# Optimization experiments

Hardware: AMD Instinct MI355X
Metric: run time of the kernel (lower is better)

Reference implementation:

```python
import jax, jax.numpy as jnp
import numpy as np

ZETA = 1.1
GAMMA = -0.1

B, F, D = 1024, 32, 128


def setup_inputs() -> dict:
    key = jax.random.key(0)
    k1, k2 = jax.random.split(key)
    feature = jax.random.normal(k1, (B, F, D), dtype=jnp.float32)
    # nn.Parameter init: normal(mean=0, std=0.001)
    matrix = jax.random.normal(k2, (F, F, D, D), dtype=jnp.float32) * 0.001
    return {"feature": feature, "matrix": matrix}


def reference(feature, matrix):
    # feature: [B, F, D]; matrix (logAlpha of hard-concrete gate): [F, F, D, D]
    nF = matrix.shape[0]
    # strict upper-triangular pair mask over (i, j)
    mask = jnp.triu(jnp.ones((nF, nF), dtype=feature.dtype), k=1)
    # deterministic (eval-mode) hard-concrete gate: stretch + clamp
    s = jax.nn.sigmoid(matrix)
    z = jnp.clip(s * (ZETA - GAMMA) + GAMMA, 0.0, 1.0)
    l0_out = mask[:, :, None, None] * z  # [F, F, D, D]
    # out[b,i,j] = f_i^T Z_ij f_j  == sum_{d,e} f[b,i,d] * Z[i,j,d,e] * f[b,j,e]
    # (faithful to: (f[:, :, None, :, None] @ f[:, None, :, None, :]) * Z, summed over (d, e))
    out = jnp.einsum('bid,ijde,bje->bij', feature, l0_out, feature)
    return out
```

## Files before the change

kernel.cpp:

```cpp
#include <hip/hip_runtime.h>

#define B_SZ 1024
#define F_SZ 32
#define D_SZ 128
#define FD   (F_SZ * D_SZ)
#define NPAIR 496

typedef __bf16 bf16x8 __attribute__((ext_vector_type(8)));
typedef __bf16 bf16x4 __attribute__((ext_vector_type(4)));
typedef float floatx4 __attribute__((ext_vector_type(4)));
typedef unsigned short u16x8 __attribute__((ext_vector_type(8)));

__device__ __forceinline__ unsigned short f2bf(float f) {
  unsigned u = __float_as_uint(f);
  u += 0x7fffu + ((u >> 16) & 1u);
  return (unsigned short)(u >> 16);
}

__device__ __forceinline__ float bf2f(unsigned short h) {
  return __uint_as_float(((unsigned)h) << 16);
}

__device__ __forceinline__ void gload_lds16(const void* g, void* l) {
  __builtin_amdgcn_global_load_lds(
      (const __attribute__((address_space(1))) unsigned int*)g,
      (__attribute__((address_space(3))) unsigned int*)l,
      16, 0, 0);
}

__global__ __launch_bounds__(256)
void prep_kernel(const float* __restrict__ feat, const float* __restrict__ mat,
                 unsigned short* __restrict__ featHi, unsigned short* __restrict__ featLo,
                 unsigned short* __restrict__ ZT, float* __restrict__ out) {
  const int bid = blockIdx.x, t = threadIdx.x;
  __shared__ unsigned short tr[128 * 72];

  if (bid < 2 * NPAIR) {
    const int pid = bid >> 1, h = bid & 1, d0 = h * 64;
    int p = pid, i = 0;
    while (p >= F_SZ - 1 - i) { p -= F_SZ - 1 - i; ++i; }
    const int j = i + 1 + p;
    const float* zp = mat + (((size_t)i * F_SZ + j) * (size_t)(D_SZ * D_SZ));
    #pragma unroll
    for (int it = 0; it < 8; ++it) {
      int idx4 = it * 256 + t;
      int dl = idx4 >> 5, e4 = (idx4 & 31) * 4;
      const float4 v = *(const float4*)(zp + (size_t)(d0 + dl) * D_SZ + e4);
      float zs[4] = {v.x, v.y, v.z, v.w};
      #pragma unroll
      for (int c = 0; c < 4; ++c) {
        float s = 1.0f / (1.0f + __expf(-zs[c]));
        float z = fminf(1.0f, fmaxf(0.0f, fmaf(s, 1.2f, -0.1f)));
        tr[(e4 + c) * 72 + dl] = f2bf(z);
      }
    }
    __syncthreads();
    #pragma unroll
    for (int it = 0; it < 4; ++it) {
      int G = it * 256 + t;
      int e = G >> 3, gl = G & 7;
      int gs = gl ^ (e & 7);
      u16x8 v = *(const u16x8*)&tr[e * 72 + gs * 8];
      *(u16x8*)&ZT[(size_t)pid * (D_SZ * D_SZ) + e * 128 + d0 + gl * 8] = v;
    }
  } else if (bid < 2 * NPAIR + 1024) {
    int idx = (bid - 2 * NPAIR) * 256 + t;
    const float4* f4 = (const float4*)feat + (size_t)idx * 4;
    #pragma unroll
    for (int q = 0; q < 2; ++q) {
      float4 a = f4[q * 2], b = f4[q * 2 + 1];
      float vs[8] = {a.x, a.y, a.z, a.w, b.x, b.y, b.z, b.w};
      u16x8 hi, lo;
      #pragma unroll
      for (int c = 0; c < 8; ++c) {
        unsigned short hh = f2bf(vs[c]);
        hi[c] = hh;
        lo[c] = f2bf(vs[c] - bf2f(hh));
      }
      *(u16x8*)&featHi[(size_t)idx * 16 + q * 8] = hi;
      *(u16x8*)&featLo[(size_t)idx * 16 + q * 8] = lo;
    }
  } else {
    int idx = (bid - (2 * NPAIR + 1024)) * 256 + t;
    float4* o4 = (float4*)out + (size_t)idx * 4;
    float4 z = {0.f, 0.f, 0.f, 0.f};
    o4[0] = z; o4[1] = z; o4[2] = z; o4[3] = z;
  }
}

__global__ __launch_bounds__(256, 3)
void interaction_pair_kernel(const unsigned short* __restrict__ featHi,
                             const unsigned short* __restrict__ featLo,
                             const unsigned short* __restrict__ ZT,
                             float* __restrict__ out) {
  __shared__ unsigned short sZ[128 * 128];
  __shared__ unsigned short sW[4 * 2048];

  const int t    = threadIdx.x;
  const int w    = t >> 6;
  const int lane = t & 63;
  const int l15  = lane & 15;
  const int quad = lane >> 4;
  const int swz  = (l15 & 7) << 4;

  const int pid   = blockIdx.x >> 3;
  const int split = blockIdx.x & 7;
  int p = pid, i = 0;
  while (p >= F_SZ - 1 - i) { p -= F_SZ - 1 - i; ++i; }
  const int j = i + 1 + p;

  {
    const char* src = (const char*)(ZT + (size_t)pid * (D_SZ * D_SZ));
    #pragma unroll
    for (int it = 0; it < 8; ++it) {
      int off = it * 4096 + w * 1024;
      gload_lds16(src + off + lane * 16, (char*)sZ + off);
    }
  }
  __syncthreads();

  const int rbase = split * 128 + w * 32;

  floatx4 acc[8][2];
  #pragma unroll
  for (int m = 0; m < 8; ++m) {
    acc[m][0] = (floatx4){0.f, 0.f, 0.f, 0.f};
    acc[m][1] = (floatx4){0.f, 0.f, 0.f, 0.f};
  }

  #pragma unroll
  for (int k0 = 0; k0 < 4; ++k0) {
    const int dq = k0 * 32 + quad * 8;
    bf16x8 b0f = *(const bf16x8*)&featHi[(size_t)(rbase +      l15) * FD + i * D_SZ + dq];
    bf16x8 b1f = *(const bf16x8*)&featHi[(size_t)(rbase + 16 + l15) * FD + i * D_SZ + dq];
    #pragma unroll
    for (int m = 0; m < 8; ++m) {
      const int e = m * 16 + l15;
      bf16x8 za = *(const bf16x8*)((const char*)sZ + e * 256 + ((2 * dq) ^ swz));
      acc[m][0] = __builtin_amdgcn_mfma_f32_16x16x32_bf16(za, b0f, acc[m][0], 0, 0, 0);
      acc[m][1] = __builtin_amdgcn_mfma_f32_16x16x32_bf16(za, b1f, acc[m][1], 0, 0, 0);
    }
  }

  char* wb = (char*)(sW + w * 2048);
  #pragma unroll
  for (int n = 0; n < 2; ++n) {
    #pragma unroll
    for (int m = 0; m < 8; ++m) {
      floatx4 c = acc[m][n];
      bf16x4 v = {(__bf16)c[0], (__bf16)c[1], (__bf16)c[2], (__bf16)c[3]};
      const int e0 = m * 16 + quad * 4;
      *(bf16x4*)(wb + l15 * 256 + ((2 * e0) ^ swz)) = v;
    }
    const int row = rbase + n * 16 + l15;
    const unsigned short* fj_h = featHi + (size_t)row * FD + j * D_SZ;
    const unsigned short* fj_l = featLo + (size_t)row * FD + j * D_SZ;
    floatx4 g = (floatx4){0.f, 0.f, 0.f, 0.f};
    #pragma unroll
    for (int k0 = 0; k0 < 4; ++k0) {
      bf16x8 wf = *(const bf16x8*)(wb + l15 * 256 + ((k0 * 64 + quad * 16) ^ swz));
      bf16x8 ah = *(const bf16x8*)(fj_h + k0 * 32 + quad * 8);
      bf16x8 al = *(const bf16x8*)(fj_l + k0 * 32 + quad * 8);
      g = __builtin_amdgcn_mfma_f32_16x16x32_bf16(ah, wf, g, 0, 0, 0);
      g = __builtin_amdgcn_mfma_f32_16x16x32_bf16(al, wf, g, 0, 0, 0);
    }
    if ((l15 >> 2) == quad) {
      const int r = l15 & 3;
      float val = g[r];
      out[(size_t)row * (F_SZ * F_SZ) + (size_t)i * F_SZ + j] = val;
    }
  }
}

extern "C" void kernel_launch(void* const* d_in, const int* in_sizes, int n_in,
                              void* d_out, int out_size, void* d_ws, size_t ws_size,
                              hipStream_t stream) {
  const float* feat = (const float*)d_in[0];
  const float* mat  = (const float*)d_in[1];
  float* out = (float*)d_out;

  unsigned short* featHi = (unsigned short*)d_ws;
  unsigned short* featLo = featHi + (size_t)B_SZ * F_SZ * D_SZ;
  unsigned short* ZT     = featLo + (size_t)B_SZ * F_SZ * D_SZ;

  const int prep_grid = 2 * NPAIR + 1024 + 256;
  prep_kernel<<<dim3(prep_grid), dim3(256), 0, stream>>>(feat, mat, featHi, featLo, ZT, out);
  interaction_pair_kernel<<<dim3(NPAIR * 8), dim3(256), 0, stream>>>(featHi, featLo, ZT, out);
}
```

Before: 158.1 us.

## Keep Z tile in registers across batch passes and finish dot product in fp32

Each block now covers 512 batch rows in four passes instead of 128, and the whole 128x128 bf16 Z tile is loaded once from LDS into registers and reused across passes. The second stage no longer rounds the intermediate to bf16, writes it to LDS and runs split hi/lo MFMAs. Instead it dots the fp32 MFMA accumulators with the fp32 feature_j directly, then reduces across lanes with shuffles. This drops the featLo workspace and the intermediate LDS buffer, at the cost of far more VGPRs (occupancy bound lowered to 2) and fewer blocks (992).

```diff
diff --git a/kernel.cpp b/kernel.cpp
--- a/kernel.cpp
+++ b/kernel.cpp
@@ -3,11 +3,10 @@
 #define B_SZ 1024
 #define F_SZ 32
 #define D_SZ 128
-#define FD   (F_SZ * D_SZ)
+#define FD   4096
 #define NPAIR 496
 
 typedef __bf16 bf16x8 __attribute__((ext_vector_type(8)));
-typedef __bf16 bf16x4 __attribute__((ext_vector_type(4)));
 typedef float floatx4 __attribute__((ext_vector_type(4)));
 typedef unsigned short u16x8 __attribute__((ext_vector_type(8)));
 
@@ -17,8 +16,8 @@
   return (unsigned short)(u >> 16);
 }
 
-__device__ __forceinline__ float bf2f(unsigned short h) {
-  return __uint_as_float(((unsigned)h) << 16);
+__device__ __forceinline__ bf16x8 as_bf16x8(floatx4 v) {
+  union { floatx4 f; bf16x8 b; } u; u.f = v; return u.b;
 }
 
 __device__ __forceinline__ void gload_lds16(const void* g, void* l) {
@@ -30,7 +29,7 @@
 
 __global__ __launch_bounds__(256)
 void prep_kernel(const float* __restrict__ feat, const float* __restrict__ mat,
-                 unsigned short* __restrict__ featHi, unsigned short* __restrict__ featLo,
+                 unsigned short* __restrict__ featB,
                  unsigned short* __restrict__ ZT, float* __restrict__ out) {
   const int bid = blockIdx.x, t = threadIdx.x;
   __shared__ unsigned short tr[128 * 72];
@@ -70,15 +69,10 @@
     for (int q = 0; q < 2; ++q) {
       float4 a = f4[q * 2], b = f4[q * 2 + 1];
       float vs[8] = {a.x, a.y, a.z, a.w, b.x, b.y, b.z, b.w};
-      u16x8 hi, lo;
+      u16x8 hi;
       #pragma unroll
-      for (int c = 0; c < 8; ++c) {
-        unsigned short hh = f2bf(vs[c]);
-        hi[c] = hh;
-        lo[c] = f2bf(vs[c] - bf2f(hh));
-      }
-      *(u16x8*)&featHi[(size_t)idx * 16 + q * 8] = hi;
-      *(u16x8*)&featLo[(size_t)idx * 16 + q * 8] = lo;
+      for (int c = 0; c < 8; ++c) hi[c] = f2bf(vs[c]);
+      *(u16x8*)&featB[(size_t)idx * 16 + q * 8] = hi;
     }
   } else {
     int idx = (bid - (2 * NPAIR + 1024)) * 256 + t;
@@ -88,13 +82,12 @@
   }
 }
 
-__global__ __launch_bounds__(256, 3)
-void interaction_pair_kernel(const unsigned short* __restrict__ featHi,
-                             const unsigned short* __restrict__ featLo,
+__global__ __launch_bounds__(256, 2)
+void interaction_pair_kernel(const float* __restrict__ feat,
+                             const unsigned short* __restrict__ featB,
                              const unsigned short* __restrict__ ZT,
                              float* __restrict__ out) {
   __shared__ unsigned short sZ[128 * 128];
-  __shared__ unsigned short sW[4 * 2048];
 
   const int t    = threadIdx.x;
   const int w    = t >> 6;
@@ -103,8 +96,8 @@
   const int quad = lane >> 4;
   const int swz  = (l15 & 7) << 4;
 
-  const int pid   = blockIdx.x >> 3;
-  const int split = blockIdx.x & 7;
+  const int pid   = blockIdx.x >> 1;
+  const int split = blockIdx.x & 1;
   int p = pid, i = 0;
   while (p >= F_SZ - 1 - i) { p -= F_SZ - 1 - i; ++i; }
   const int j = i + 1 + p;
@@ -119,55 +112,52 @@
   }
   __syncthreads();
 
-  const int rbase = split * 128 + w * 32;
+  floatx4 zr[4][8];
+  #pragma unroll
+  for (int k0 = 0; k0 < 4; ++k0)
+    #pragma unroll
+    for (int m = 0; m < 8; ++m)
+      zr[k0][m] = *(const floatx4*)((const char*)sZ + (m * 16 + l15) * 256 +
+                                    ((k0 * 64 + quad * 16) ^ swz));
+  #pragma unroll
+  for (int k0 = 0; k0 < 4; ++k0)
+    #pragma unroll
+    for (int m = 0; m < 8; ++m)
+      asm volatile("" : "+v"(zr[k0][m]));
 
-  floatx4 acc[8][2];
-  #pragma unroll
-  for (int m = 0; m < 8; ++m) {
-    acc[m][0] = (floatx4){0.f, 0.f, 0.f, 0.f};
-    acc[m][1] = (floatx4){0.f, 0.f, 0.f, 0.f};
-  }
+  #pragma unroll 1
+  for (int pass = 0; pass < 4; ++pass) {
+    const int rbase = split * 512 + pass * 128 + w * 32;
 
-  #pragma unroll
-  for (int k0 = 0; k0 < 4; ++k0) {
-    const int dq = k0 * 32 + quad * 8;
-    bf16x8 b0f = *(const bf16x8*)&featHi[(size_t)(rbase +      l15) * FD + i * D_SZ + dq];
-    bf16x8 b1f = *(const bf16x8*)&featHi[(size_t)(rbase + 16 + l15) * FD + i * D_SZ + dq];
     #pragma unroll
-    for (int m = 0; m < 8; ++m) {
-      const int e = m * 16 + l15;
-      bf16x8 za = *(const bf16x8*)((const char*)sZ + e * 256 + ((2 * dq) ^ swz));
-      acc[m][0] = __builtin_amdgcn_mfma_f32_16x16x32_bf16(za, b0f, acc[m][0], 0, 0, 0);
-      acc[m][1] = __builtin_amdgcn_mfma_f32_16x16x32_bf16(za, b1f, acc[m][1], 0, 0, 0);
-    }
-  }
+    for (int n = 0; n < 2; ++n) {
+      const int row = rbase + n * 16 + l15;
 
-  char* wb = (char*)(sW + w * 2048);
-  #pragma unroll
-  for (int n = 0; n < 2; ++n) {
-    #pragma unroll
-    for (int m = 0; m < 8; ++m) {
-      floatx4 c = acc[m][n];
-      bf16x4 v = {(__bf16)c[0], (__bf16)c[1], (__bf16)c[2], (__bf16)c[3]};
-      const int e0 = m * 16 + quad * 4;
-      *(bf16x4*)(wb + l15 * 256 + ((2 * e0) ^ swz)) = v;
-    }
-    const int row = rbase + n * 16 + l15;
-    const unsigned short* fj_h = featHi + (size_t)row * FD + j * D_SZ;
-    const unsigned short* fj_l = featLo + (size_t)row * FD + j * D_SZ;
-    floatx4 g = (floatx4){0.f, 0.f, 0.f, 0.f};
-    #pragma unroll
-    for (int k0 = 0; k0 < 4; ++k0) {
-      bf16x8 wf = *(const bf16x8*)(wb + l15 * 256 + ((k0 * 64 + quad * 16) ^ swz));
-      bf16x8 ah = *(const bf16x8*)(fj_h + k0 * 32 + quad * 8);
-      bf16x8 al = *(const bf16x8*)(fj_l + k0 * 32 + quad * 8);
-      g = __builtin_amdgcn_mfma_f32_16x16x32_bf16(ah, wf, g, 0, 0, 0);
-      g = __builtin_amdgcn_mfma_f32_16x16x32_bf16(al, wf, g, 0, 0, 0);
-    }
-    if ((l15 >> 2) == quad) {
-      const int r = l15 & 3;
-      float val = g[r];
-      out[(size_t)row * (F_SZ * F_SZ) + (size_t)i * F_SZ + j] = val;
+      floatx4 a8[8];
+      #pragma unroll
+      for (int m = 0; m < 8; ++m) a8[m] = (floatx4){0.f, 0.f, 0.f, 0.f};
+
+      const unsigned short* bp = featB + (size_t)row * FD + i * D_SZ + quad * 8;
+      #pragma unroll
+      for (int k0 = 0; k0 < 4; ++k0) {
+        bf16x8 bf = *(const bf16x8*)(bp + k0 * 32);
+        #pragma unroll
+        for (int m = 0; m < 8; ++m)
+          a8[m] = __builtin_amdgcn_mfma_f32_16x16x32_bf16(
+              as_bf16x8(zr[k0][m]), bf, a8[m], 0, 0, 0);
+      }
+
+      float pl = 0.f;
+      const float* fp = feat + (size_t)row * FD + j * D_SZ + quad * 4;
+      #pragma unroll
+      for (int m = 0; m < 8; ++m) {
+        const float4 f4 = *(const float4*)(fp + m * 16);
+        pl += a8[m][0] * f4.x + a8[m][1] * f4.y + a8[m][2] * f4.z + a8[m][3] * f4.w;
+      }
+      pl += __shfl_xor(pl, 16, 64);
+      pl += __shfl_xor(pl, 32, 64);
+      if (quad == 0)
+        out[(size_t)row * (F_SZ * F_SZ) + (size_t)i * F_SZ + j] = pl;
     }
   }
 }
@@ -179,11 +169,10 @@
   const float* mat  = (const float*)d_in[1];
   float* out = (float*)d_out;
 
-  unsigned short* featHi = (unsigned short*)d_ws;
-  unsigned short* featLo = featHi + (size_t)B_SZ * F_SZ * D_SZ;
-  unsigned short* ZT     = featLo + (size_t)B_SZ * F_SZ * D_SZ;
+  unsigned short* featB = (unsigned short*)d_ws;
+  unsigned short* ZT    = featB + (size_t)B_SZ * F_SZ * D_SZ;
 
   const int prep_grid = 2 * NPAIR + 1024 + 256;
-  prep_kernel<<<dim3(prep_grid), dim3(256), 0, stream>>>(feat, mat, featHi, featLo, ZT, out);
-  interaction_pair_kernel<<<dim3(NPAIR * 8), dim3(256), 0, stream>>>(featHi, featLo, ZT, out);
+  prep_kernel<<<dim3(prep_grid), dim3(256), 0, stream>>>(feat, mat, featB, ZT, out);
+  interaction_pair_kernel<<<dim3(NPAIR * 2), dim3(256), 0, stream>>>(feat, featB, ZT, out);
 }
```

Measured after the change: 154.2 us. 2.4% less time.
